# Optimization experiments

Measured on AMD Instinct MI355X. Metric: run time of the kernel, lower is better.

## Reference

```python
import jax, jax.numpy as jnp
import numpy as np
import math

D = 1024      # model dim
H = 16        # heads
DK = D // H   # 64
FF = 4096     # ff_dim
B, T = 2, 2048


def _norm(x, alpha, bias, eps=1e-6):
    # torch: (x - mean) / (x.std(unbiased) + eps) * alpha + bias
    mu = jnp.mean(x, axis=-1, keepdims=True)
    sd = jnp.std(x, axis=-1, keepdims=True, ddof=1)  # unbiased, like torch
    return alpha * ((x - mu) / (sd + eps)) + bias


def setup_inputs() -> dict:
    key = jax.random.key(0)
    ks = jax.random.split(key, 20)
    w = lambda k, shp: (jax.random.normal(k, shp, jnp.float32) * 0.02)
    inp = {
        "x": jax.random.normal(ks[0], (B, T, D), jnp.float32),
        "x_mask": jnp.ones((B, T), jnp.int32),  # unused by the module's forward
        "Wq": w(ks[1], (D, D)), "bq": jnp.zeros((D,), jnp.float32),
        "Wk": w(ks[2], (D, D)), "bk": jnp.zeros((D,), jnp.float32),
        "Wv": w(ks[3], (D, D)), "bv": jnp.zeros((D,), jnp.float32),
        "Wo": w(ks[4], (D, D)), "bo": jnp.zeros((D,), jnp.float32),
        "W1": w(ks[5], (D, FF)), "b1": jnp.zeros((FF,), jnp.float32),
        "W2": w(ks[6], (FF, D)), "b2": jnp.zeros((D,), jnp.float32),
        "alpha1": jnp.ones((D,), jnp.float32), "beta1": jnp.zeros((D,), jnp.float32),
        "alpha2": jnp.ones((D,), jnp.float32), "beta2": jnp.zeros((D,), jnp.float32),
    }
    return inp


def reference(x, x_mask, Wq, bq, Wk, bk, Wv, bv, Wo, bo,
              W1, b1, W2, b2, alpha1, beta1, alpha2, beta2):
    b, t, d = x.shape
    # projections -> [B, H, T, DK]
    q = (x @ Wq + bq).reshape(b, t, H, DK).swapaxes(1, 2)
    k = (x @ Wk + bk).reshape(b, t, H, DK).swapaxes(1, 2)
    v = (x @ Wv + bv).reshape(b, t, H, DK).swapaxes(1, 2)
    # eager attention: QK^T / sqrt(dk), clamp_min(-6000), softmax (no mask used)
    score = jnp.einsum('bhqd,bhkd->bhqk', q, k) / math.sqrt(DK)
    score = jnp.maximum(score, -6000.0)
    score = jax.nn.softmax(score, axis=-1)  # dropout=identity at inference
    val = jnp.einsum('bhqk,bhkd->bhqd', score, v)
    val = val.swapaxes(1, 2).reshape(b, t, d)
    attn_out = val @ Wo + bo
    # residual + norm1 (dropout identity)
    xn = _norm(x + attn_out, alpha1, beta1)
    # FFN: relu(linear1) -> linear2
    ff = jnp.maximum(xn @ W1 + b1, 0.0) @ W2 + b2
    out = _norm(xn + ff, alpha2, beta2)
    return out, score
```

## Files before the change

### kernel.cpp

```cpp
#include <hip/hip_runtime.h>
#include <stdint.h>

#define T_SEQ   2048
#define D_MODEL 1024
#define N_HEADS 16
#define D_HEAD  64
#define FF_DIM  4096
#define BATCH   2
#define BT      (BATCH * T_SEQ)

typedef unsigned short u16;
typedef __attribute__((ext_vector_type(8))) short bf16x8;
typedef __attribute__((ext_vector_type(4))) float f32x4;

__device__ __forceinline__ u16 f2bf(float f) {
  union { float f; unsigned u; } x; x.f = f;
  unsigned r = x.u + 0x7fffu + ((x.u >> 16) & 1u);
  return (u16)(r >> 16);
}

__device__ __forceinline__ void gload16(const void* g, void* l) {
  __builtin_amdgcn_global_load_lds(
      (const __attribute__((address_space(1))) void*)g,
      (__attribute__((address_space(3))) void*)l, 16, 0, 0);
}

struct PrepArgs {
  const float* x; u16* xb;
  const float *Wq, *Wk, *Wv, *Wo, *W1, *W2;
  u16 *WqT, *WkT, *WvT, *WoT, *W1T, *W2T;
};

__global__ __launch_bounds__(256)
void prep_kernel(PrepArgs pa) {
  const int bid = blockIdx.x;
  const int tid = threadIdx.x;
  if (bid < 4096) {
    int i = (bid * 256 + tid) * 4;
    float4 v = *(const float4*)(pa.x + i);
    ushort4 o; o.x = f2bf(v.x); o.y = f2bf(v.y); o.z = f2bf(v.z); o.w = f2bf(v.w);
    *(ushort4*)(pa.xb + i) = o;
    return;
  }
  int t = bid - 4096;
  const float* W; u16* Wt; int K, N, rel;
  if (t < 1024)      { W = pa.Wq; Wt = pa.WqT; K = 1024; N = 1024; rel = t; }
  else if (t < 2048) { W = pa.Wk; Wt = pa.WkT; K = 1024; N = 1024; rel = t - 1024; }
  else if (t < 3072) { W = pa.Wv; Wt = pa.WvT; K = 1024; N = 1024; rel = t - 2048; }
  else if (t < 4096) { W = pa.Wo; Wt = pa.WoT; K = 1024; N = 1024; rel = t - 3072; }
  else if (t < 8192) { W = pa.W1; Wt = pa.W1T; K = 1024; N = 4096; rel = t - 4096; }
  else               { W = pa.W2; Wt = pa.W2T; K = 4096; N = 1024; rel = t - 8192; }
  const int ntn = N >> 5;
  const int n0 = (rel % ntn) * 32, k0 = (rel / ntn) * 32;
  const int tx = tid & 31, ty = tid >> 5;
  __shared__ float tile[32][33];
#pragma unroll
  for (int r = 0; r < 4; ++r)
    tile[ty + r * 8][tx] = W[(size_t)(k0 + ty + r * 8) * N + n0 + tx];
  __syncthreads();
#pragma unroll
  for (int r = 0; r < 4; ++r)
    Wt[(size_t)(n0 + ty + r * 8) * K + k0 + tx] = f2bf(tile[tx][ty + r * 8]);
}

struct GemmArgs {
  const u16* A;
  const u16* B0; const u16* B1; const u16* B2;
  const float* bias0; const float* bias1; const float* bias2;
  void* out0; void* out1; void* out2;
  int M, N, K;
};

template <int EPI>
__global__ __launch_bounds__(256, 2)
void gemm_bt(GemmArgs ga) {
  const int tid = threadIdx.x;
  const int gx = gridDim.x, gy = gridDim.y;
  const int nwg = gx * gy * gridDim.z;
  const int orig = blockIdx.x + gx * (blockIdx.y + gy * blockIdx.z);
  const int swz = (orig & 7) * (nwg >> 3) + (orig >> 3);
  const int bx = swz % gx, by = (swz / gx) % gy, bz = swz / (gx * gy);
  const int m0 = by * 128;
  const int n0 = bx * 128;
  const int lane = tid & 63, w = tid >> 6;
  const int wr = w >> 1, wc = w & 1;
  const int l15 = lane & 15, g = lane >> 4;

  const u16* Bt; const float* bias; void* outp;
  int z = 0;
  if (EPI == 0) {
    z = bz;
    Bt   = (z == 0) ? ga.B0   : (z == 1) ? ga.B1   : ga.B2;
    bias = (z == 0) ? ga.bias0 : (z == 1) ? ga.bias1 : ga.bias2;
    outp = (z == 0) ? ga.out0 : (z == 1) ? ga.out1 : ga.out2;
  } else if (EPI == 3) {
    z = bz; Bt = ga.B0; bias = nullptr; outp = ga.out0;
  } else { Bt = ga.B0; bias = ga.bias0; outp = ga.out0; }

  __shared__ char lsA[128 * 128];
  __shared__ char lsB[128 * 128];

  f32x4 acc[4][4] = {};
  const int K = ga.K;
  const int kbase = (EPI == 3) ? z * (K >> 1) : 0;
  const int nk = (EPI == 3) ? (K >> 7) : (K >> 6);

  auto stage = [&](int kt) {
    const int k0 = kbase + kt * 64;
#pragma unroll
    for (int i = 0; i < 4; ++i) {
      int o = i * 4096 + tid * 16;
      int row = o >> 7, cb = o & 127;
      int lcb = cb ^ ((row & 7) << 4);
      gload16((const char*)ga.A + ((size_t)(m0 + row) * K + k0) * 2 + lcb, lsA + o);
    }
#pragma unroll
    for (int i = 0; i < 4; ++i) {
      int o = i * 4096 + tid * 16;
      int row = o >> 7, cb = o & 127;
      int lcb = cb ^ ((row & 7) << 4);
      gload16((const char*)Bt + ((size_t)(n0 + row) * K + k0) * 2 + lcb, lsB + o);
    }
  };

  stage(0);
  for (int kt = 0; kt < nk; ++kt) {
    __syncthreads();
#pragma unroll
    for (int kk = 0; kk < 2; ++kk) {
      bf16x8 a[4], b[4];
#pragma unroll
      for (int mi = 0; mi < 4; ++mi) {
        int row = wr * 64 + mi * 16 + l15;
        a[mi] = *(const bf16x8*)(lsA + row * 128 + ((kk * 64 + g * 16) ^ ((row & 7) << 4)));
      }
#pragma unroll
      for (int ni = 0; ni < 4; ++ni) {
        int row = wc * 64 + ni * 16 + l15;
        b[ni] = *(const bf16x8*)(lsB + row * 128 + ((kk * 64 + g * 16) ^ ((row & 7) << 4)));
      }
#pragma unroll
      for (int mi = 0; mi < 4; ++mi)
#pragma unroll
        for (int ni = 0; ni < 4; ++ni)
          acc[mi][ni] = __builtin_amdgcn_mfma_f32_16x16x32_bf16(a[mi], b[ni], acc[mi][ni], 0, 0, 0);
    }
    __syncthreads();
    if (kt + 1 < nk) stage(kt + 1);
  }

  const int N = ga.N;
#pragma unroll
  for (int mi = 0; mi < 4; ++mi) {
#pragma unroll
    for (int ni = 0; ni < 4; ++ni) {
      const int c = n0 + wc * 64 + ni * 16 + l15;
      const float bv = (EPI == 3) ? 0.0f : bias[c];
#pragma unroll
      for (int j = 0; j < 4; ++j) {
        const int r = m0 + wr * 64 + mi * 16 + g * 4 + j;
        float v = acc[mi][ni][j] + bv;
        if constexpr (EPI == 0) {
          const int bb = r >> 11, t = r & 2047, hh = c >> 6, dk = c & 63;
          u16* o = (u16*)outp;
          size_t idx = (z < 2)
              ? ((size_t)((bb * N_HEADS + hh) * T_SEQ + t)) * D_HEAD + dk
              : ((size_t)((bb * N_HEADS + hh) * D_HEAD + dk)) * T_SEQ + t;
          o[idx] = f2bf(v);
        } else if constexpr (EPI == 3) {
          ((float*)outp)[(size_t)z * ga.M * N + (size_t)r * N + c] = v;
        } else {
          ((u16*)outp)[(size_t)r * N + c] = f2bf(fmaxf(v, 0.0f));
        }
      }
    }
  }
}

__global__ __launch_bounds__(256, 2)
void attn_kernel(const u16* __restrict__ q, const u16* __restrict__ k,
                 const u16* __restrict__ vT, float* __restrict__ score,
                 u16* __restrict__ val) {
  const int tid = threadIdx.x;
  const int lane = tid & 63, w = tid >> 6;
  const int l15 = lane & 15, g = lane >> 4;
  const int nwg = gridDim.x;
  const int orig = blockIdx.x;
  const int swz = (orig & 7) * (nwg >> 3) + (orig >> 3);
  const int bh = swz >> 5;
  const int Q0 = (swz & 31) * 64;
  const size_t hoff = (size_t)bh * T_SEQ * D_HEAD;
  const u16* qb = q + hoff;
  const u16* kb = k + hoff;
  const u16* vb = vT + hoff;
  float* sb = score + ((size_t)bh * T_SEQ + Q0) * T_SEQ;

  __shared__ char lsK[128 * 128];
  __shared__ char lsV[64 * 256];
  __shared__ char lsP[4][16 * 256];

  bf16x8 qf[2];
  {
    int row = Q0 + w * 16 + l15;
#pragma unroll
    for (int kk = 0; kk < 2; ++kk)
      qf[kk] = *(const bf16x8*)(qb + (size_t)row * D_HEAD + kk * 32 + g * 8);
  }

  float lsum[4] = {0.f, 0.f, 0.f, 0.f};

  for (int jt = 0; jt < 16; ++jt) {
    const int J0 = jt * 128;
    __syncthreads();
#pragma unroll
    for (int i = 0; i < 4; ++i) {
      int o = i * 4096 + tid * 16;
      int row = o >> 7, cb = o & 127;
      int lcb = cb ^ ((row & 7) << 4);
      gload16((const char*)kb + ((size_t)(J0 + row) * D_HEAD) * 2 + lcb, lsK + o);
    }
    __syncthreads();
#pragma unroll
    for (int nt = 0; nt < 8; ++nt) {
      f32x4 s = {0.f, 0.f, 0.f, 0.f};
#pragma unroll
      for (int kk = 0; kk < 2; ++kk) {
        int row = nt * 16 + l15;
        bf16x8 bfr = *(const bf16x8*)(lsK + row * 128 + ((kk * 64 + g * 16) ^ ((row & 7) << 4)));
        s = __builtin_amdgcn_mfma_f32_16x16x32_bf16(qf[kk], bfr, s, 0, 0, 0);
      }
#pragma unroll
      for (int j = 0; j < 4; ++j) {
        float sv = fmaxf(s[j] * 0.125f, -6000.0f);
        lsum[j] += __expf(sv);
      }
    }
  }
#pragma unroll
  for (int j = 0; j < 4; ++j) {
    float v = lsum[j];
    v += __shfl_xor(v, 1);
    v += __shfl_xor(v, 2);
    v += __shfl_xor(v, 4);
    v += __shfl_xor(v, 8);
    lsum[j] = 1.0f / v;
  }

  f32x4 vacc[4] = {};

  for (int jt = 0; jt < 16; ++jt) {
    const int J0 = jt * 128;
    __syncthreads();
#pragma unroll
    for (int i = 0; i < 4; ++i) {
      int o = i * 4096 + tid * 16;
      int row = o >> 7, cb = o & 127;
      int lcb = cb ^ ((row & 7) << 4);
      gload16((const char*)kb + ((size_t)(J0 + row) * D_HEAD) * 2 + lcb, lsK + o);
    }
#pragma unroll
    for (int i = 0; i < 4; ++i) {
      int o = i * 4096 + tid * 16;
      int row = o >> 8, cb = o & 255;
      int lcb = cb ^ ((row & 7) << 4);
      gload16((const char*)vb + ((size_t)row * T_SEQ + J0) * 2 + lcb, lsV + o);
    }
    __syncthreads();
    char* myP = lsP[w];
#pragma unroll
    for (int nt = 0; nt < 8; ++nt) {
      f32x4 s = {0.f, 0.f, 0.f, 0.f};
#pragma unroll
      for (int kk = 0; kk < 2; ++kk) {
        int row = nt * 16 + l15;
        bf16x8 bfr = *(const bf16x8*)(lsK + row * 128 + ((kk * 64 + g * 16) ^ ((row & 7) << 4)));
        s = __builtin_amdgcn_mfma_f32_16x16x32_bf16(qf[kk], bfr, s, 0, 0, 0);
      }
#pragma unroll
      for (int j = 0; j < 4; ++j) {
        float sv = fmaxf(s[j] * 0.125f, -6000.0f);
        float p = __expf(sv) * lsum[j];
        int qr = 4 * g + j;
        __builtin_nontemporal_store(p, &sb[(size_t)(w * 16 + qr) * T_SEQ + J0 + nt * 16 + l15]);
        int colb = (nt * 16 + l15) * 2;
        *(u16*)(myP + qr * 256 + (colb ^ ((qr & 7) << 4))) = f2bf(p);
      }
    }
#pragma unroll
    for (int ks = 0; ks < 4; ++ks) {
      bf16x8 pa = *(const bf16x8*)(myP + l15 * 256 + ((ks * 64 + g * 16) ^ ((l15 & 7) << 4)));
#pragma unroll
      for (int nt2 = 0; nt2 < 4; ++nt2) {
        int vrow = nt2 * 16 + l15;
        bf16x8 vf = *(const bf16x8*)(lsV + vrow * 256 + ((ks * 64 + g * 16) ^ ((vrow & 7) << 4)));
        vacc[nt2] = __builtin_amdgcn_mfma_f32_16x16x32_bf16(pa, vf, vacc[nt2], 0, 0, 0);
      }
    }
  }

  const int bb = bh >> 4, hh = bh & 15;
#pragma unroll
  for (int nt2 = 0; nt2 < 4; ++nt2)
#pragma unroll
    for (int j = 0; j < 4; ++j) {
      int qr = w * 16 + 4 * g + j;
      int dk = nt2 * 16 + l15;
      val[((size_t)(bb * T_SEQ + Q0 + qr)) * D_MODEL + hh * D_HEAD + dk] = f2bf(vacc[nt2][j]);
    }
}

template <bool WRITE_BF16>
__global__ __launch_bounds__(256)
void norm_kernel(const float* __restrict__ p0, const float* __restrict__ p1,
                 const float* __restrict__ bias, const float* __restrict__ resid,
                 const float* __restrict__ alpha, const float* __restrict__ beta,
                 float* __restrict__ outf, u16* __restrict__ outb) {
  const int row = blockIdx.x;
  const int tid = threadIdx.x;
  const size_t base = (size_t)row * D_MODEL + tid * 4;
  float4 v0 = *(const float4*)(p0 + base);
  float4 v1 = *(const float4*)(p1 + base);
  float4 bi = *(const float4*)(bias + tid * 4);
  float4 rs = *(const float4*)(resid + base);
  float4 v;
  v.x = v0.x + v1.x + bi.x + rs.x;
  v.y = v0.y + v1.y + bi.y + rs.y;
  v.z = v0.z + v1.z + bi.z + rs.z;
  v.w = v0.w + v1.w + bi.w + rs.w;
  float s = v.x + v.y + v.z + v.w;
  float ss = v.x * v.x + v.y * v.y + v.z * v.z + v.w * v.w;
#pragma unroll
  for (int m = 1; m < 64; m <<= 1) {
    s += __shfl_xor(s, m);
    ss += __shfl_xor(ss, m);
  }
  __shared__ float red[8];
  int w = tid >> 6, lane = tid & 63;
  if (lane == 0) { red[w] = s; red[4 + w] = ss; }
  __syncthreads();
  s = red[0] + red[1] + red[2] + red[3];
  ss = red[4] + red[5] + red[6] + red[7];
  float mu = s * (1.0f / 1024.0f);
  float var = fmaxf(ss - s * mu, 0.0f) * (1.0f / 1023.0f);
  float inv = 1.0f / (sqrtf(var) + 1e-6f);
  float4 a = *(const float4*)(alpha + tid * 4);
  float4 be = *(const float4*)(beta + tid * 4);
  float4 o;
  o.x = (v.x - mu) * inv * a.x + be.x;
  o.y = (v.y - mu) * inv * a.y + be.y;
  o.z = (v.z - mu) * inv * a.z + be.z;
  o.w = (v.w - mu) * inv * a.w + be.w;
  *(float4*)(outf + base) = o;
  if (WRITE_BF16) {
    ushort4 ob; ob.x = f2bf(o.x); ob.y = f2bf(o.y); ob.z = f2bf(o.z); ob.w = f2bf(o.w);
    *(ushort4*)(outb + base) = ob;
  }
}

extern "C" void kernel_launch(void* const* d_in, const int* in_sizes, int n_in,
                              void* d_out, int out_size, void* d_ws, size_t ws_size,
                              hipStream_t stream) {
  const float* x   = (const float*)d_in[0];
  const float* Wq  = (const float*)d_in[2];
  const float* bq  = (const float*)d_in[3];
  const float* Wk  = (const float*)d_in[4];
  const float* bk  = (const float*)d_in[5];
  const float* Wv  = (const float*)d_in[6];
  const float* bv  = (const float*)d_in[7];
  const float* Wo  = (const float*)d_in[8];
  const float* bo  = (const float*)d_in[9];
  const float* W1  = (const float*)d_in[10];
  const float* b1  = (const float*)d_in[11];
  const float* W2  = (const float*)d_in[12];
  const float* b2  = (const float*)d_in[13];
  const float* a1  = (const float*)d_in[14];
  const float* be1 = (const float*)d_in[15];
  const float* a2  = (const float*)d_in[16];
  const float* be2 = (const float*)d_in[17];

  float* out   = (float*)d_out;
  float* score = out + (size_t)BT * D_MODEL;

  char* ws = (char*)d_ws;
  const size_t MB = (size_t)1 << 20;
  u16*   xb   = (u16*)(ws + 0 * MB);
  u16*   WqT  = (u16*)(ws + 8 * MB);
  u16*   WkT  = (u16*)(ws + 10 * MB);
  u16*   WvT  = (u16*)(ws + 12 * MB);
  u16*   WoT  = (u16*)(ws + 14 * MB);
  u16*   W1T  = (u16*)(ws + 16 * MB);
  u16*   W2T  = (u16*)(ws + 24 * MB);
  u16*   qw   = (u16*)(ws + 32 * MB);
  u16*   kw   = (u16*)(ws + 40 * MB);
  u16*   vTw  = (u16*)(ws + 48 * MB);
  u16*   valw = (u16*)(ws + 56 * MB);
  float* p0   = (float*)(ws + 64 * MB);
  float* p1   = (float*)(ws + 80 * MB);
  float* xn   = (float*)(ws + 0 * MB);
  u16*   xnb  = (u16*)(ws + 96 * MB);
  u16*   hw   = (u16*)(ws + 32 * MB);

  {
    PrepArgs pa{ x, xb, Wq, Wk, Wv, Wo, W1, W2, WqT, WkT, WvT, WoT, W1T, W2T };
    prep_kernel<<<16384, 256, 0, stream>>>(pa);
  }

  {
    GemmArgs ga{};
    ga.A = xb;
    ga.B0 = WqT; ga.B1 = WkT; ga.B2 = WvT;
    ga.bias0 = bq; ga.bias1 = bk; ga.bias2 = bv;
    ga.out0 = qw; ga.out1 = kw; ga.out2 = vTw;
    ga.M = BT; ga.N = D_MODEL; ga.K = D_MODEL;
    gemm_bt<0><<<dim3(8, 32, 3), 256, 0, stream>>>(ga);
  }

  attn_kernel<<<1024, 256, 0, stream>>>(qw, kw, vTw, score, valw);

  {
    GemmArgs ga{};
    ga.A = valw; ga.B0 = WoT; ga.out0 = p0;
    ga.M = BT; ga.N = D_MODEL; ga.K = D_MODEL;
    gemm_bt<3><<<dim3(8, 32, 2), 256, 0, stream>>>(ga);
  }

  norm_kernel<true><<<BT, 256, 0, stream>>>(p0, p0 + (size_t)BT * D_MODEL, bo, x,
                                            a1, be1, xn, xnb);

  {
    GemmArgs ga{};
    ga.A = xnb; ga.B0 = W1T; ga.bias0 = b1; ga.out0 = hw;
    ga.M = BT; ga.N = FF_DIM; ga.K = D_MODEL;
    gemm_bt<2><<<dim3(32, 32, 1), 256, 0, stream>>>(ga);
  }

  {
    GemmArgs ga{};
    ga.A = hw; ga.B0 = W2T; ga.out0 = p0;
    ga.M = BT; ga.N = D_MODEL; ga.K = FF_DIM;
    gemm_bt<3><<<dim3(8, 32, 2), 256, 0, stream>>>(ga);
  }

  norm_kernel<false><<<BT, 256, 0, stream>>>(p0, p0 + (size_t)BT * D_MODEL, b2, xn,
                                             a2, be2, out, nullptr);
}
```

Measured before the change: 370.5 us.

## Load K and V fragments directly from global in attention, drop LDS staging

The attention kernel stops staging K and V tiles in shared memory and reads the MFMA operand fragments straight from global memory (through L1/L2), which removes the block-wide barriers per tile. The shared-memory footprint shrinks to the per-wave P buffer, so launch bounds are raised to three blocks per CU, and MFMA sections are wrapped in s_setprio. Each wave now issues its own redundant global loads for K/V with no cross-wave reuse, so more cache traffic and load latency may be exposed.

After: 570.7 us. +54.0%, slower.

```diff
diff --git a/kernel.cpp b/kernel.cpp
--- a/kernel.cpp
+++ b/kernel.cpp
@@ -177,7 +177,7 @@
   }
 }
 
-__global__ __launch_bounds__(256, 2)
+__global__ __launch_bounds__(256, 3)
 void attn_kernel(const u16* __restrict__ q, const u16* __restrict__ k,
                  const u16* __restrict__ vT, float* __restrict__ score,
                  u16* __restrict__ val) {
@@ -195,8 +195,6 @@
   const u16* vb = vT + hoff;
   float* sb = score + ((size_t)bh * T_SEQ + Q0) * T_SEQ;
 
-  __shared__ char lsK[128 * 128];
-  __shared__ char lsV[64 * 256];
   __shared__ char lsP[4][16 * 256];
 
   bf16x8 qf[2];
@@ -211,24 +209,16 @@
 
   for (int jt = 0; jt < 16; ++jt) {
     const int J0 = jt * 128;
-    __syncthreads();
-#pragma unroll
-    for (int i = 0; i < 4; ++i) {
-      int o = i * 4096 + tid * 16;
-      int row = o >> 7, cb = o & 127;
-      int lcb = cb ^ ((row & 7) << 4);
-      gload16((const char*)kb + ((size_t)(J0 + row) * D_HEAD) * 2 + lcb, lsK + o);
-    }
-    __syncthreads();
 #pragma unroll
     for (int nt = 0; nt < 8; ++nt) {
       f32x4 s = {0.f, 0.f, 0.f, 0.f};
+      __builtin_amdgcn_s_setprio(1);
 #pragma unroll
       for (int kk = 0; kk < 2; ++kk) {
-        int row = nt * 16 + l15;
-        bf16x8 bfr = *(const bf16x8*)(lsK + row * 128 + ((kk * 64 + g * 16) ^ ((row & 7) << 4)));
+        bf16x8 bfr = *(const bf16x8*)(kb + (size_t)(J0 + nt * 16 + l15) * D_HEAD + kk * 32 + g * 8);
         s = __builtin_amdgcn_mfma_f32_16x16x32_bf16(qf[kk], bfr, s, 0, 0, 0);
       }
+      __builtin_amdgcn_s_setprio(0);
 #pragma unroll
       for (int j = 0; j < 4; ++j) {
         float sv = fmaxf(s[j] * 0.125f, -6000.0f);
@@ -247,35 +237,20 @@
   }
 
   f32x4 vacc[4] = {};
+  char* myP = lsP[w];
 
   for (int jt = 0; jt < 16; ++jt) {
     const int J0 = jt * 128;
-    __syncthreads();
-#pragma unroll
-    for (int i = 0; i < 4; ++i) {
-      int o = i * 4096 + tid * 16;
-      int row = o >> 7, cb = o & 127;
-      int lcb = cb ^ ((row & 7) << 4);
-      gload16((const char*)kb + ((size_t)(J0 + row) * D_HEAD) * 2 + lcb, lsK + o);
-    }
-#pragma unroll
-    for (int i = 0; i < 4; ++i) {
-      int o = i * 4096 + tid * 16;
-      int row = o >> 8, cb = o & 255;
-      int lcb = cb ^ ((row & 7) << 4);
-      gload16((const char*)vb + ((size_t)row * T_SEQ + J0) * 2 + lcb, lsV + o);
-    }
-    __syncthreads();
-    char* myP = lsP[w];
 #pragma unroll
     for (int nt = 0; nt < 8; ++nt) {
       f32x4 s = {0.f, 0.f, 0.f, 0.f};
+      __builtin_amdgcn_s_setprio(1);
 #pragma unroll
       for (int kk = 0; kk < 2; ++kk) {
-        int row = nt * 16 + l15;
-        bf16x8 bfr = *(const bf16x8*)(lsK + row * 128 + ((kk * 64 + g * 16) ^ ((row & 7) << 4)));
+        bf16x8 bfr = *(const bf16x8*)(kb + (size_t)(J0 + nt * 16 + l15) * D_HEAD + kk * 32 + g * 8);
         s = __builtin_amdgcn_mfma_f32_16x16x32_bf16(qf[kk], bfr, s, 0, 0, 0);
       }
+      __builtin_amdgcn_s_setprio(0);
 #pragma unroll
       for (int j = 0; j < 4; ++j) {
         float sv = fmaxf(s[j] * 0.125f, -6000.0f);
@@ -289,12 +264,13 @@
 #pragma unroll
     for (int ks = 0; ks < 4; ++ks) {
       bf16x8 pa = *(const bf16x8*)(myP + l15 * 256 + ((ks * 64 + g * 16) ^ ((l15 & 7) << 4)));
+      __builtin_amdgcn_s_setprio(1);
 #pragma unroll
       for (int nt2 = 0; nt2 < 4; ++nt2) {
-        int vrow = nt2 * 16 + l15;
-        bf16x8 vf = *(const bf16x8*)(lsV + vrow * 256 + ((ks * 64 + g * 16) ^ ((vrow & 7) << 4)));
+        bf16x8 vf = *(const bf16x8*)(vb + (size_t)(nt2 * 16 + l15) * T_SEQ + J0 + ks * 32 + g * 8);
         vacc[nt2] = __builtin_amdgcn_mfma_f32_16x16x32_bf16(pa, vf, vacc[nt2], 0, 0, 0);
       }
+      __builtin_amdgcn_s_setprio(0);
     }
   }
 
```

## Double-buffer K/V tiles in attention kernel and raise MFMA wave priority

Applied to the files above, without the earlier changes.

The attention kernel now keeps two LDS buffers for the K and V tiles. The next tile's global-to-LDS loads are issued before computing on the current tile, with one barrier per iteration instead of two. It also raises wave priority around the MFMA sequences with s_setprio. The aim is to hide global load latency behind compute. In exchange, LDS use per block grows, which may limit occupancy, and the kernel is likely dominated by the large score-matrix writes anyway.

New measurement: 377.9 us. 2.0% more time.

```diff
diff --git a/kernel.cpp b/kernel.cpp
--- a/kernel.cpp
+++ b/kernel.cpp
@@ -195,46 +195,64 @@
   const u16* vb = vT + hoff;
   float* sb = score + ((size_t)bh * T_SEQ + Q0) * T_SEQ;
 
-  __shared__ char lsK[128 * 128];
-  __shared__ char lsV[64 * 256];
+  __shared__ char lsK[2][128 * 128];
+  __shared__ char lsV[2][64 * 256];
   __shared__ char lsP[4][16 * 256];
 
-  bf16x8 qf[2];
-  {
-    int row = Q0 + w * 16 + l15;
-#pragma unroll
-    for (int kk = 0; kk < 2; ++kk)
-      qf[kk] = *(const bf16x8*)(qb + (size_t)row * D_HEAD + kk * 32 + g * 8);
-  }
-
-  float lsum[4] = {0.f, 0.f, 0.f, 0.f};
-
-  for (int jt = 0; jt < 16; ++jt) {
+  auto stageK = [&](int jt, char* dst) {
     const int J0 = jt * 128;
-    __syncthreads();
 #pragma unroll
     for (int i = 0; i < 4; ++i) {
       int o = i * 4096 + tid * 16;
       int row = o >> 7, cb = o & 127;
       int lcb = cb ^ ((row & 7) << 4);
-      gload16((const char*)kb + ((size_t)(J0 + row) * D_HEAD) * 2 + lcb, lsK + o);
-    }
-    __syncthreads();
+      gload16((const char*)kb + ((size_t)(J0 + row) * D_HEAD) * 2 + lcb, dst + o);
+    }
+  };
+  auto stageV = [&](int jt, char* dst) {
+    const int J0 = jt * 128;
+#pragma unroll
+    for (int i = 0; i < 4; ++i) {
+      int o = i * 4096 + tid * 16;
+      int row = o >> 8, cb = o & 255;
+      int lcb = cb ^ ((row & 7) << 4);
+      gload16((const char*)vb + ((size_t)row * T_SEQ + J0) * 2 + lcb, dst + o);
+    }
+  };
+
+  bf16x8 qf[2];
+  {
+    int row = Q0 + w * 16 + l15;
+#pragma unroll
+    for (int kk = 0; kk < 2; ++kk)
+      qf[kk] = *(const bf16x8*)(qb + (size_t)row * D_HEAD + kk * 32 + g * 8);
+  }
+
+  float lsum[4] = {0.f, 0.f, 0.f, 0.f};
+
+  stageK(0, lsK[0]);
+  __syncthreads();
+  for (int jt = 0; jt < 16; ++jt) {
+    const char* kbuf = lsK[jt & 1];
+    if (jt + 1 < 16) stageK(jt + 1, lsK[(jt + 1) & 1]);
 #pragma unroll
     for (int nt = 0; nt < 8; ++nt) {
       f32x4 s = {0.f, 0.f, 0.f, 0.f};
+      __builtin_amdgcn_s_setprio(1);
 #pragma unroll
       for (int kk = 0; kk < 2; ++kk) {
         int row = nt * 16 + l15;
-        bf16x8 bfr = *(const bf16x8*)(lsK + row * 128 + ((kk * 64 + g * 16) ^ ((row & 7) << 4)));
+        bf16x8 bfr = *(const bf16x8*)(kbuf + row * 128 + ((kk * 64 + g * 16) ^ ((row & 7) << 4)));
         s = __builtin_amdgcn_mfma_f32_16x16x32_bf16(qf[kk], bfr, s, 0, 0, 0);
       }
+      __builtin_amdgcn_s_setprio(0);
 #pragma unroll
       for (int j = 0; j < 4; ++j) {
         float sv = fmaxf(s[j] * 0.125f, -6000.0f);
         lsum[j] += __expf(sv);
       }
     }
+    __syncthreads();
   }
 #pragma unroll
   for (int j = 0; j < 4; ++j) {
@@ -247,35 +265,30 @@
   }
 
   f32x4 vacc[4] = {};
-
+  char* myP = lsP[w];
+
+  stageK(0, lsK[0]);
+  stageV(0, lsV[0]);
+  __syncthreads();
   for (int jt = 0; jt < 16; ++jt) {
     const int J0 = jt * 128;
-    __syncthreads();
-#pragma unroll
-    for (int i = 0; i < 4; ++i) {
-      int o = i * 4096 + tid * 16;
-      int row = o >> 7, cb = o & 127;
-      int lcb = cb ^ ((row & 7) << 4);
-      gload16((const char*)kb + ((size_t)(J0 + row) * D_HEAD) * 2 + lcb, lsK + o);
-    }
-#pragma unroll
-    for (int i = 0; i < 4; ++i) {
-      int o = i * 4096 + tid * 16;
-      int row = o >> 8, cb = o & 255;
-      int lcb = cb ^ ((row & 7) << 4);
-      gload16((const char*)vb + ((size_t)row * T_SEQ + J0) * 2 + lcb, lsV + o);
-    }
-    __syncthreads();
-    char* myP = lsP[w];
+    const char* kbuf = lsK[jt & 1];
+    const char* vbuf = lsV[jt & 1];
+    if (jt + 1 < 16) {
+      stageK(jt + 1, lsK[(jt + 1) & 1]);
+      stageV(jt + 1, lsV[(jt + 1) & 1]);
+    }
 #pragma unroll
     for (int nt = 0; nt < 8; ++nt) {
       f32x4 s = {0.f, 0.f, 0.f, 0.f};
+      __builtin_amdgcn_s_setprio(1);
 #pragma unroll
       for (int kk = 0; kk < 2; ++kk) {
         int row = nt * 16 + l15;
-        bf16x8 bfr = *(const bf16x8*)(lsK + row * 128 + ((kk * 64 + g * 16) ^ ((row & 7) << 4)));
+        bf16x8 bfr = *(const bf16x8*)(kbuf + row * 128 + ((kk * 64 + g * 16) ^ ((row & 7) << 4)));
         s = __builtin_amdgcn_mfma_f32_16x16x32_bf16(qf[kk], bfr, s, 0, 0, 0);
       }
+      __builtin_amdgcn_s_setprio(0);
 #pragma unroll
       for (int j = 0; j < 4; ++j) {
         float sv = fmaxf(s[j] * 0.125f, -6000.0f);
@@ -289,13 +302,16 @@
 #pragma unroll
     for (int ks = 0; ks < 4; ++ks) {
       bf16x8 pa = *(const bf16x8*)(myP + l15 * 256 + ((ks * 64 + g * 16) ^ ((l15 & 7) << 4)));
+      __builtin_amdgcn_s_setprio(1);
 #pragma unroll
       for (int nt2 = 0; nt2 < 4; ++nt2) {
         int vrow = nt2 * 16 + l15;
-        bf16x8 vf = *(const bf16x8*)(lsV + vrow * 256 + ((ks * 64 + g * 16) ^ ((vrow & 7) << 4)));
+        bf16x8 vf = *(const bf16x8*)(vbuf + vrow * 256 + ((ks * 64 + g * 16) ^ ((vrow & 7) << 4)));
         vacc[nt2] = __builtin_amdgcn_mfma_f32_16x16x32_bf16(pa, vf, vacc[nt2], 0, 0, 0);
       }
-    }
+      __builtin_amdgcn_s_setprio(0);
+    }
+    __syncthreads();
   }
 
   const int bb = bh >> 4, hh = bh & 15;
```
